# Optimization experiments

Hardware: AMD Instinct MI355X
Metric: run time of the kernel (lower is better)

The kernel has to match this reference:

```python
import jax, jax.numpy as jnp
import numpy as np

N_NODES = 50000
N_EDGES = 800000
LATDIM = 128
HEAD = 4


def setup_inputs() -> dict:
    key = jax.random.key(0)
    k1, k2, k3, k4, k5, k6 = jax.random.split(key, 6)
    scale = 1.0 / np.sqrt(LATDIM)  # xavier-ish scale for the square projections
    return {
        "embeds": jax.random.normal(k1, (N_NODES, LATDIM), dtype=jnp.float32),
        "qW": jax.random.normal(k2, (LATDIM, LATDIM), dtype=jnp.float32) * scale,
        "kW": jax.random.normal(k3, (LATDIM, LATDIM), dtype=jnp.float32) * scale,
        "vW": jax.random.normal(k4, (LATDIM, LATDIM), dtype=jnp.float32) * scale,
        "rows": jax.random.randint(k5, (N_EDGES,), 0, N_NODES, dtype=jnp.int32),
        "cols": jax.random.randint(k6, (N_EDGES,), 0, N_NODES, dtype=jnp.int32),
    }


def reference(embeds, qW, kW, vW, rows, cols):
    n_nodes, latdim = embeds.shape
    head_dim = latdim // HEAD
    rowEmb = embeds[rows]                         # [E, D] gather by dst
    colEmb = embeds[cols]                         # [E, D] gather by src
    q = (rowEmb @ qW).reshape(-1, HEAD, head_dim)  # [E, H, Dh]
    k = (colEmb @ kW).reshape(-1, HEAD, head_dim)
    v = (colEmb @ vW).reshape(-1, HEAD, head_dim)
    att = jnp.einsum('ehd,ehd->eh', q, k)
    att = jnp.clip(att, -10.0, 10.0)
    expAtt = jnp.exp(att)                          # [E, H]
    # segment softmax denominator via scatter-add over destination nodes
    attNorm = jax.ops.segment_sum(expAtt, rows, num_segments=n_nodes)[rows]
    att = expAtt / (attNorm + 1e-8)
    res = (att[:, :, None] * v).reshape(-1, latdim)  # [E, D]
    out = jax.ops.segment_sum(res, rows, num_segments=n_nodes)  # [N, D]
    return out
```

## Files before the change

### kernel.cpp

```cpp
#include <hip/hip_runtime.h>
#include <hip/hip_bf16.h>

#define N_NODES 50000
#define N_EDGES 800000
#define LATDIM 128
#define HEAD 4
#define SLOT_CAP 96

typedef __attribute__((ext_vector_type(8))) short short8;
typedef __attribute__((ext_vector_type(8))) _Float16 half8;
typedef __attribute__((ext_vector_type(4))) float floatx4;

__device__ __forceinline__ unsigned bf16_rne_bits(float x) {
    unsigned u = __builtin_bit_cast(unsigned, x);
    return (u + 0x7fffu + ((u >> 16) & 1u)) & 0xffff0000u;
}
__device__ __forceinline__ void split_bf16(float x, short& hi, short& lo) {
    unsigned hb = bf16_rne_bits(x);
    hi = (short)(hb >> 16);
    float hf = __builtin_bit_cast(float, hb);
    unsigned lb = bf16_rne_bits(x - hf);
    lo = (short)(lb >> 16);
}

__global__ __launch_bounds__(256) void init_kernel(
    const float* __restrict__ qW, const float* __restrict__ kW,
    const float* __restrict__ vW,
    short* __restrict__ Whi, short* __restrict__ Wlo,
    int* __restrict__ cnt)
{
    const int b = blockIdx.x;
    if (b < 192) {
        const int which = b >> 6;
        const float* W = (which == 0) ? qW : (which == 1) ? kW : vW;
        const int t = (b & 63) * 256 + threadIdx.x;
        const int k = t >> 7, n = t & 127;
        const int c = k >> 5, q = (k >> 3) & 3, j = k & 7;
        short hi, lo;
        split_bf16(W[k * 128 + n], hi, lo);
        const int dst = which * 16384 + ((c * 128 + n) * 4 + q) * 8 + j;
        Whi[dst] = hi;
        Wlo[dst] = lo;
    } else {
        const int t = (b - 192) * 256 + threadIdx.x;
        if (t < N_NODES) cnt[t] = 0;
    }
}

#define SCAT_UNITS ((N_EDGES / 4 + 255) / 256)
#define GEMM_TILES ((N_NODES + 31) / 32)
#define TOTAL_BLOCKS (3 * SCAT_UNITS)
#define LDSP 136

__global__ __launch_bounds__(256) void gemm_scatter_kernel(
    const float* __restrict__ E,
    const short* __restrict__ Whi, const short* __restrict__ Wlo,
    const int* __restrict__ rows, const int* __restrict__ cols,
    int* __restrict__ cnt, int* __restrict__ slots,
    float* __restrict__ Q, unsigned short* __restrict__ KV2)
{
    __shared__ short AhL[32 * LDSP];
    __shared__ short AlL[32 * LDSP];
    __shared__ unsigned short Stage[32 * 256];

    const int b = blockIdx.x;
    const int r3 = b % 3;

    if (r3 == 0) {
        const int t = (b / 3) * 256 + threadIdx.x;
        if (t < N_EDGES / 4) {
            int4 r = ((const int4*)rows)[t];
            int4 c = ((const int4*)cols)[t];
            int p;
            p = atomicAdd(&cnt[r.x], 1);
            if (p < SLOT_CAP) slots[(size_t)r.x * SLOT_CAP + p] = c.x;
            p = atomicAdd(&cnt[r.y], 1);
            if (p < SLOT_CAP) slots[(size_t)r.y * SLOT_CAP + p] = c.y;
            p = atomicAdd(&cnt[r.z], 1);
            if (p < SLOT_CAP) slots[(size_t)r.z * SLOT_CAP + p] = c.z;
            p = atomicAdd(&cnt[r.w], 1);
            if (p < SLOT_CAP) slots[(size_t)r.w * SLOT_CAP + p] = c.w;
        }
        return;
    }

    const int tile = 2 * (b / 3) + (r3 - 1);
    if (tile >= GEMM_TILES) return;
    const int r_base = tile * 32;

#pragma unroll 4
    for (int chnk = threadIdx.x; chnk < 1024; chnk += 256) {
        const int row = chnk >> 5, c4 = chnk & 31;
        int grow = r_base + row;
        if (grow > N_NODES - 1) grow = N_NODES - 1;
        float4 x = ((const float4*)E)[(size_t)grow * 32 + c4];
        short h0, l0, h1, l1, h2, l2, h3, l3;
        split_bf16(x.x, h0, l0);
        split_bf16(x.y, h1, l1);
        split_bf16(x.z, h2, l2);
        split_bf16(x.w, h3, l3);
        *(short4*)(AhL + row * LDSP + c4 * 4) = make_short4(h0, h1, h2, h3);
        *(short4*)(AlL + row * LDSP + c4 * 4) = make_short4(l0, l1, l2, l3);
    }
    __syncthreads();

    const int wave = threadIdx.x >> 6;
    const int lane = threadIdx.x & 63;
    const int n_base = wave * 32;
    const int ln = lane & 15;
    const int q  = lane >> 4;

#pragma unroll 1
    for (int which = 1; which < 3; ++which) {
        const int vs = (which == 2) ? 32 : 0;
#pragma unroll 1
        for (int tIdx = 0; tIdx < 2; ++tIdx) {
            short8 Bh[4], Bl[4];
#pragma unroll
            for (int c = 0; c < 4; ++c) {
                const int off = which * 16384 +
                                ((c * 128 + n_base + tIdx * 16 + ln) * 4 + q) * 8;
                Bh[c] = *(const short8*)(Whi + off);
                Bl[c] = *(const short8*)(Wlo + off);
            }

#pragma unroll
            for (int rt = 0; rt < 2; ++rt) {
                const short* ah = AhL + (rt * 16 + ln) * LDSP + q * 8;
                const short* al = AlL + (rt * 16 + ln) * LDSP + q * 8;
                floatx4 acc = {0.f, 0.f, 0.f, 0.f};
#pragma unroll
                for (int c = 0; c < 4; ++c) {
                    short8 Ah = *(const short8*)(ah + c * 32);
                    short8 Al = *(const short8*)(al + c * 32);
                    acc = __builtin_amdgcn_mfma_f32_16x16x32_bf16(Ah, Bh[c], acc, 0, 0, 0);
                    acc = __builtin_amdgcn_mfma_f32_16x16x32_bf16(Ah, Bl[c], acc, 0, 0, 0);
                    acc = __builtin_amdgcn_mfma_f32_16x16x32_bf16(Al, Bh[c], acc, 0, 0, 0);
                }
#pragma unroll
                for (int r = 0; r < 4; ++r) {
                    const int lr = rt * 16 + q * 4 + r;
                    Stage[lr * 256 + wave * 64 + tIdx * 16 + ln + vs] =
                        __builtin_bit_cast(unsigned short, (_Float16)acc[r]);
                }
            }
        }
    }
    __syncthreads();

#pragma unroll
    for (int it = 0; it < 4; ++it) {
        const int ch = threadIdx.x + it * 256;
        const int lr = ch >> 5;
        if (r_base + lr < N_NODES)
            ((uint4*)(KV2 + (size_t)r_base * 256))[ch] = ((const uint4*)Stage)[ch];
    }
    __syncthreads();

    {
        const int which = 0;
        float* QS = (float*)Stage;
#pragma unroll 1
        for (int tIdx = 0; tIdx < 2; ++tIdx) {
            short8 Bh[4], Bl[4];
#pragma unroll
            for (int c = 0; c < 4; ++c) {
                const int off = which * 16384 +
                                ((c * 128 + n_base + tIdx * 16 + ln) * 4 + q) * 8;
                Bh[c] = *(const short8*)(Whi + off);
                Bl[c] = *(const short8*)(Wlo + off);
            }
            const int cc = n_base + tIdx * 16 + ln;

#pragma unroll
            for (int rt = 0; rt < 2; ++rt) {
                const short* ah = AhL + (rt * 16 + ln) * LDSP + q * 8;
                const short* al = AlL + (rt * 16 + ln) * LDSP + q * 8;
                floatx4 acc = {0.f, 0.f, 0.f, 0.f};
#pragma unroll
                for (int c = 0; c < 4; ++c) {
                    short8 Ah = *(const short8*)(ah + c * 32);
                    short8 Al = *(const short8*)(al + c * 32);
                    acc = __builtin_amdgcn_mfma_f32_16x16x32_bf16(Ah, Bh[c], acc, 0, 0, 0);
                    acc = __builtin_amdgcn_mfma_f32_16x16x32_bf16(Ah, Bl[c], acc, 0, 0, 0);
                    acc = __builtin_amdgcn_mfma_f32_16x16x32_bf16(Al, Bh[c], acc, 0, 0, 0);
                }
#pragma unroll
                for (int r = 0; r < 4; ++r) {
                    const int lr = rt * 16 + q * 4 + r;
                    QS[lr * 128 + cc] = acc[r];
                }
            }
        }
    }
    __syncthreads();

#pragma unroll
    for (int it = 0; it < 4; ++it) {
        const int ch = threadIdx.x + it * 256;
        const int lr = ch >> 5;
        if (r_base + lr < N_NODES)
            ((float4*)(Q + (size_t)r_base * 128))[ch] = ((const float4*)Stage)[ch];
    }
}

__global__ __launch_bounds__(256) void fused_kernel(
    const float* __restrict__ Q,
    const unsigned short* __restrict__ KV2,
    const int* __restrict__ cnt,
    const int* __restrict__ slots,
    float* __restrict__ out)
{
    const int n = blockIdx.x * 4 + (threadIdx.x >> 6);
    if (n >= N_NODES) return;
    const int lane = threadIdx.x & 63;
    const int s  = lane & 1;
    const int h  = (lane >> 1) & 3;
    const int el = lane >> 3;

    int deg = cnt[n];
    if (deg > SLOT_CAP) deg = SLOT_CAP;

    float qv[16];
    {
        const float4* qp = (const float4*)(Q + (size_t)n * 128 + h * 32 + s * 16);
#pragma unroll
        for (int j = 0; j < 4; ++j) {
            float4 t = qp[j];
            qv[4 * j + 0] = t.x; qv[4 * j + 1] = t.y;
            qv[4 * j + 2] = t.z; qv[4 * j + 3] = t.w;
        }
    }

    float acc[16];
#pragma unroll
    for (int j = 0; j < 16; ++j) acc[j] = 0.f;
    float norm = 0.f;

    const int* srow = slots + (size_t)n * SLOT_CAP;

    for (int i = 0; i < deg; i += 8) {
        const int e = i + el;
        if (e < deg) {
            const int col = srow[e];
            const _Float16* kp = (const _Float16*)(KV2 + (size_t)col * 256 + h * 64 + s * 16);
            half8 k0 = *(const half8*)(kp);
            half8 k1 = *(const half8*)(kp + 8);
            half8 v0 = *(const half8*)(kp + 32);
            half8 v1 = *(const half8*)(kp + 40);

            float p = 0.f;
#pragma unroll
            for (int d = 0; d < 8; ++d) {
                p = fmaf((float)k0[d], qv[d], p);
                p = fmaf((float)k1[d], qv[8 + d], p);
            }
            p += __shfl_xor(p, 1);

            float a = __expf(fminf(fmaxf(p, -10.0f), 10.0f));
            norm += a;

#pragma unroll
            for (int d = 0; d < 8; ++d) {
                acc[d]     = fmaf((float)v0[d], a, acc[d]);
                acc[8 + d] = fmaf((float)v1[d], a, acc[8 + d]);
            }
        }
    }

#pragma unroll
    for (int m = 8; m <= 32; m <<= 1) {
        norm += __shfl_xor(norm, m, 64);
#pragma unroll
        for (int j = 0; j < 16; ++j) acc[j] += __shfl_xor(acc[j], m, 64);
    }

    if (el == 0) {
        const float inv = 1.0f / (norm + 1e-8f);
        float4* op = (float4*)(out + (size_t)n * 128 + h * 32 + s * 16);
#pragma unroll
        for (int j = 0; j < 4; ++j)
            op[j] = make_float4(acc[4 * j] * inv, acc[4 * j + 1] * inv,
                                acc[4 * j + 2] * inv, acc[4 * j + 3] * inv);
    }
}

extern "C" void kernel_launch(void* const* d_in, const int* in_sizes, int n_in,
                              void* d_out, int out_size, void* d_ws, size_t ws_size,
                              hipStream_t stream) {
    const float* embeds = (const float*)d_in[0];
    const float* qW     = (const float*)d_in[1];
    const float* kW     = (const float*)d_in[2];
    const float* vW     = (const float*)d_in[3];
    const int*   rows   = (const int*)d_in[4];
    const int*   cols   = (const int*)d_in[5];
    float* out = (float*)d_out;

    float* Q = (float*)d_ws;
    unsigned short* KV2 = (unsigned short*)(Q + (size_t)N_NODES * LATDIM);
    int* cnt   = (int*)(KV2 + (size_t)N_NODES * 256);
    int* slots = cnt + N_NODES;
    short* Whi = (short*)(slots + (size_t)N_NODES * SLOT_CAP);
    short* Wlo = Whi + 3 * 16384;

    init_kernel<<<192 + (N_NODES + 255) / 256, 256, 0, stream>>>(
        qW, kW, vW, Whi, Wlo, cnt);

    gemm_scatter_kernel<<<TOTAL_BLOCKS, 256, 0, stream>>>(
        embeds, Whi, Wlo, rows, cols, cnt, slots, Q, KV2);

    fused_kernel<<<(N_NODES + 3) / 4, 256, 0, stream>>>(
        Q, KV2, cnt, slots, out);
}
```

Before: 193.4 us.

## Replace global atomic edge scatter with two-pass bucketed binning

```diff
diff --git a/kernel.cpp b/kernel.cpp
--- a/kernel.cpp
+++ b/kernel.cpp
@@ -6,6 +6,11 @@
 #define LATDIM 128
 #define HEAD 4
 #define SLOT_CAP 96
+
+#define BUCKETS 196
+#define BCAP 4608
+#define A_BLOCKS 98
+#define A_CHUNKS 2048
 
 typedef __attribute__((ext_vector_type(8))) short short8;
 typedef __attribute__((ext_vector_type(8))) _Float16 half8;
@@ -27,7 +32,8 @@
     const float* __restrict__ qW, const float* __restrict__ kW,
     const float* __restrict__ vW,
     short* __restrict__ Whi, short* __restrict__ Wlo,
-    int* __restrict__ cnt)
+    const int* __restrict__ rows, const int* __restrict__ cols,
+    int* __restrict__ alloc, unsigned* __restrict__ binned)
 {
     const int b = blockIdx.x;
     if (b < 192) {
@@ -41,51 +47,95 @@
         const int dst = which * 16384 + ((c * 128 + n) * 4 + q) * 8 + j;
         Whi[dst] = hi;
         Wlo[dst] = lo;
-    } else {
-        const int t = (b - 192) * 256 + threadIdx.x;
-        if (t < N_NODES) cnt[t] = 0;
-    }
-}
-
-#define SCAT_UNITS ((N_EDGES / 4 + 255) / 256)
+        return;
+    }
+
+    __shared__ int hist[BUCKETS];
+    __shared__ int base[BUCKETS];
+    const int ab = b - 192;
+
+    for (int t = threadIdx.x; t < BUCKETS; t += 256) hist[t] = 0;
+    __syncthreads();
+
+#pragma unroll 1
+    for (int it = 0; it < 8; ++it) {
+        const int ch = ab * A_CHUNKS + it * 256 + threadIdx.x;
+        if (ch < N_EDGES / 4) {
+            int4 r = ((const int4*)rows)[ch];
+            atomicAdd(&hist[r.x >> 8], 1);
+            atomicAdd(&hist[r.y >> 8], 1);
+            atomicAdd(&hist[r.z >> 8], 1);
+            atomicAdd(&hist[r.w >> 8], 1);
+        }
+    }
+    __syncthreads();
+
+    for (int t = threadIdx.x; t < BUCKETS; t += 256) {
+        base[t] = atomicAdd(&alloc[t], hist[t]);
+        hist[t] = 0;
+    }
+    __syncthreads();
+
+#pragma unroll 1
+    for (int it = 0; it < 8; ++it) {
+        const int ch = ab * A_CHUNKS + it * 256 + threadIdx.x;
+        if (ch < N_EDGES / 4) {
+            int4 r = ((const int4*)rows)[ch];
+            int4 c = ((const int4*)cols)[ch];
+            int bk, p;
+            bk = r.x >> 8; p = base[bk] + atomicAdd(&hist[bk], 1);
+            if (p < BCAP) binned[(size_t)bk * BCAP + p] =
+                ((unsigned)(r.x & 255) << 16) | (unsigned)c.x;
+            bk = r.y >> 8; p = base[bk] + atomicAdd(&hist[bk], 1);
+            if (p < BCAP) binned[(size_t)bk * BCAP + p] =
+                ((unsigned)(r.y & 255) << 16) | (unsigned)c.y;
+            bk = r.z >> 8; p = base[bk] + atomicAdd(&hist[bk], 1);
+            if (p < BCAP) binned[(size_t)bk * BCAP + p] =
+                ((unsigned)(r.z & 255) << 16) | (unsigned)c.z;
+            bk = r.w >> 8; p = base[bk] + atomicAdd(&hist[bk], 1);
+            if (p < BCAP) binned[(size_t)bk * BCAP + p] =
+                ((unsigned)(r.w & 255) << 16) | (unsigned)c.w;
+        }
+    }
+}
+
 #define GEMM_TILES ((N_NODES + 31) / 32)
-#define TOTAL_BLOCKS (3 * SCAT_UNITS)
+#define TOTAL_BLOCKS (BUCKETS + GEMM_TILES)
 #define LDSP 136
 
-__global__ __launch_bounds__(256) void gemm_scatter_kernel(
+__global__ __launch_bounds__(256) void gemm_place_kernel(
     const float* __restrict__ E,
     const short* __restrict__ Whi, const short* __restrict__ Wlo,
-    const int* __restrict__ rows, const int* __restrict__ cols,
+    const int* __restrict__ alloc, const unsigned* __restrict__ binned,
     int* __restrict__ cnt, int* __restrict__ slots,
     float* __restrict__ Q, unsigned short* __restrict__ KV2)
 {
     __shared__ short AhL[32 * LDSP];
     __shared__ short AlL[32 * LDSP];
     __shared__ unsigned short Stage[32 * 256];
+    __shared__ int cl[256];
 
     const int b = blockIdx.x;
-    const int r3 = b % 3;
-
-    if (r3 == 0) {
-        const int t = (b / 3) * 256 + threadIdx.x;
-        if (t < N_EDGES / 4) {
-            int4 r = ((const int4*)rows)[t];
-            int4 c = ((const int4*)cols)[t];
-            int p;
-            p = atomicAdd(&cnt[r.x], 1);
-            if (p < SLOT_CAP) slots[(size_t)r.x * SLOT_CAP + p] = c.x;
-            p = atomicAdd(&cnt[r.y], 1);
-            if (p < SLOT_CAP) slots[(size_t)r.y * SLOT_CAP + p] = c.y;
-            p = atomicAdd(&cnt[r.z], 1);
-            if (p < SLOT_CAP) slots[(size_t)r.z * SLOT_CAP + p] = c.z;
-            p = atomicAdd(&cnt[r.w], 1);
-            if (p < SLOT_CAP) slots[(size_t)r.w * SLOT_CAP + p] = c.w;
-        }
+
+    if (b < BUCKETS) {
+        cl[threadIdx.x] = 0;
+        __syncthreads();
+        const int nrec = min(alloc[b], BCAP);
+        const unsigned* rec = binned + (size_t)b * BCAP;
+        for (int i = threadIdx.x; i < nrec; i += 256) {
+            const unsigned rc = rec[i];
+            const int rl = rc >> 16;
+            const int p = atomicAdd(&cl[rl], 1);
+            if (p < SLOT_CAP)
+                slots[(size_t)(b * 256 + rl) * SLOT_CAP + p] = (int)(rc & 0xffffu);
+        }
+        __syncthreads();
+        const int node = b * 256 + threadIdx.x;
+        if (node < N_NODES) cnt[node] = cl[threadIdx.x];
         return;
     }
 
-    const int tile = 2 * (b / 3) + (r3 - 1);
-    if (tile >= GEMM_TILES) return;
+    const int tile = b - BUCKETS;
     const int r_base = tile * 32;
 
 #pragma unroll 4
@@ -302,12 +352,16 @@
     int* slots = cnt + N_NODES;
     short* Whi = (short*)(slots + (size_t)N_NODES * SLOT_CAP);
     short* Wlo = Whi + 3 * 16384;
-
-    init_kernel<<<192 + (N_NODES + 255) / 256, 256, 0, stream>>>(
-        qW, kW, vW, Whi, Wlo, cnt);
-
-    gemm_scatter_kernel<<<TOTAL_BLOCKS, 256, 0, stream>>>(
-        embeds, Whi, Wlo, rows, cols, cnt, slots, Q, KV2);
+    int* alloc = (int*)(Wlo + 3 * 16384);
+    unsigned* binned = (unsigned*)(alloc + BUCKETS);
+
+    hipMemsetAsync(alloc, 0, sizeof(int) * BUCKETS, stream);
+
+    init_kernel<<<192 + A_BLOCKS, 256, 0, stream>>>(
+        qW, kW, vW, Whi, Wlo, rows, cols, alloc, binned);
+
+    gemm_place_kernel<<<TOTAL_BLOCKS, 256, 0, stream>>>(
+        embeds, Whi, Wlo, alloc, binned, cnt, slots, Q, KV2);
 
     fused_kernel<<<(N_NODES + 3) / 4, 256, 0, stream>>>(
         Q, KV2, cnt, slots, out);
```

Measured after the change: 185.8 us. 1.04x faster.
